# Kernel optimization log

Hardware: AMD Instinct MI355X
Metric: run time of the kernel (lower is better)

Reference implementation:

```python
import jax, jax.numpy as jnp
import numpy as np

TEMPERATURE = 0.6
REPETITION_PENALTY = 1.2
VOCAB = 50257


def setup_inputs() -> dict:
    key = jax.random.key(0)
    k1, k2 = jax.random.split(key)
    logits = jax.random.normal(k1, (8, 64, VOCAB), dtype=jnp.float32)
    prev_tokens = jax.random.randint(k2, (64, 200), 0, VOCAB, dtype=jnp.int64)
    return {"logits": logits, "prev_tokens": prev_tokens}


def reference(logits, prev_tokens):
    # logits: [B, S, V]; prev_tokens: [S, P] token ids previously generated per sequence.
    B, S, V = logits.shape
    # set-semantics mask of penalized (seq, token) pairs; duplicate ids collapse to one.
    mask = jnp.zeros((S, V), dtype=bool).at[
        jnp.arange(S)[:, None], prev_tokens
    ].set(True)  # [S, V]
    # torch.all over dim 0: penalty multiplies if all batch logits negative, else divides.
    all_neg = jnp.all(logits < 0, axis=0, keepdims=True)  # [1, S, V]
    penalized = jnp.where(all_neg, logits * REPETITION_PENALTY, logits / REPETITION_PENALTY)
    logits = jnp.where(mask[None, :, :], penalized, logits)
    # Categorical(logits=x) -> probs = softmax(x); temperature scaling fused.
    return jax.nn.softmax(logits / TEMPERATURE, axis=-1)
```

## Files before the change

kernel.cpp:

```cpp
#include <hip/hip_runtime.h>
#include <math.h>

#define BB 8
#define SS 64
#define VV 50257
#define PP 200
#define NMASK 1571
#define NT 1024
#define ITER 13
constexpr float RP   = 1.2f;
constexpr float TINV = 1.0f / 0.6f;

__global__ __launch_bounds__(NT) void sch_fused_kernel(
        const float* __restrict__ logits,
        const int*   __restrict__ prev,
        float*       __restrict__ out) {
    __shared__ unsigned mask[NMASK];
    __shared__ float ss[16];
    __shared__ float bc_li;

    const int bs  = blockIdx.x;
    const int s   = bs & (SS - 1);
    const int tid = threadIdx.x;
    const float* row  = logits + (size_t)bs * VV;
    float*       orow = out    + (size_t)bs * VV;

    for (int i = tid; i < NMASK; i += NT) mask[i] = 0u;
    __syncthreads();

    float delta  = 0.0f;
    float eadj   = 0.0f;
    int   vtok   = -1;
    bool  winner = false;
    if (tid < PP) {
        vtok = prev[s * PP + tid];
        unsigned bit = 1u << (vtok & 31);
        unsigned old = atomicOr(&mask[vtok >> 5], bit);
        winner = (old & bit) == 0u;
        if (winner) {
            float lv[BB];
            bool all_neg = true;
            #pragma unroll
            for (int b = 0; b < BB; ++b) {
                lv[b] = logits[((size_t)(b * SS + s)) * VV + vtok];
                all_neg = all_neg && (lv[b] < 0.0f);
            }
            const float myraw = lv[bs >> 6];
            const float adj   = all_neg ? myraw * RP : myraw / RP;
            eadj  = __expf(adj * TINV);
            delta = eadj - __expf(myraw * TINV);
        }
    }

    const int a0   = (4 - (bs & 3)) & 3;
    const int nb   = (VV - a0) >> 2;
    const int tail = VV - a0 - (nb << 2);
    const int tstart = a0 + (nb << 2);

    const float4* body = (const float4*)(row + a0);
    float4 buf[ITER];
    #pragma unroll
    for (int k = 0; k < ITER; ++k) {
        int i = tid + k * NT;
        if (i < nb) buf[k] = body[i];
    }
    float escal = 0.0f;
    const bool has_head = (tid < a0);
    const bool has_tail = (tid >= 4 && tid < 4 + tail);
    if (has_head) escal = __expf(row[tid] * TINV);
    if (has_tail) escal = __expf(row[tstart + tid - 4] * TINV);

    float4 acc = make_float4(0.f, 0.f, 0.f, 0.f);
    #pragma unroll
    for (int k = 0; k < ITER; ++k) {
        int i = tid + k * NT;
        if (i < nb) {
            float4 x = buf[k];
            float4 e;
            e.x = __expf(x.x * TINV);
            e.y = __expf(x.y * TINV);
            e.z = __expf(x.z * TINV);
            e.w = __expf(x.w * TINV);
            buf[k] = e;
            acc.x += e.x; acc.y += e.y; acc.z += e.z; acc.w += e.w;
        }
    }
    float sum = (acc.x + acc.y) + (acc.z + acc.w) + escal + delta;

    #pragma unroll
    for (int off = 1; off < 64; off <<= 1)
        sum += __shfl_xor(sum, off);
    const int wave = tid >> 6, lane = tid & 63;
    if (lane == 0) ss[wave] = sum;
    __syncthreads();
    if (tid == 0) {
        float S0 = ss[0];
        #pragma unroll
        for (int w = 1; w < 16; ++w) S0 += ss[w];
        bc_li = 1.0f / S0;
    }
    __syncthreads();
    const float li = bc_li;

    float4* obody = (float4*)(orow + a0);
    #pragma unroll
    for (int k = 0; k < ITER; ++k) {
        int i = tid + k * NT;
        if (i < nb) {
            float4 e = buf[k];
            obody[i] = make_float4(e.x * li, e.y * li, e.z * li, e.w * li);
        }
    }
    if (has_head) orow[tid]               = escal * li;
    if (has_tail) orow[tstart + tid - 4]  = escal * li;

    __syncthreads();
    if (winner) orow[vtok] = eadj * li;
}

extern "C" void kernel_launch(void* const* d_in, const int* in_sizes, int n_in,
                              void* d_out, int out_size, void* d_ws, size_t ws_size,
                              hipStream_t stream) {
    const float* logits = (const float*)d_in[0];
    const int*   prev   = (const int*)d_in[1];
    float* out = (float*)d_out;

    sch_fused_kernel<<<BB * SS, NT, 0, stream>>>(logits, prev, out);
}
```

Measured before the change: 187.3 us.

## Hoist row and penalty-token loads before mask setup, use nontemporal output stores

Issues the bulk row loads and the eight gathered batch logits per previous token before the mask clear and atomic dedup, so their latency overlaps the shared-memory setup and barrier. Output writes now use nontemporal stores to avoid polluting cache with streaming data. The launch bounds gain a min-blocks hint and float4 is replaced by an ext_vector type. The gathers now run for every token thread rather than only dedup winners, which adds redundant loads, and the occupancy hint may constrain register allocation.

```diff
diff --git a/kernel.cpp b/kernel.cpp
--- a/kernel.cpp
+++ b/kernel.cpp
@@ -11,7 +11,9 @@
 constexpr float RP   = 1.2f;
 constexpr float TINV = 1.0f / 0.6f;
 
-__global__ __launch_bounds__(NT) void sch_fused_kernel(
+typedef float f32x4 __attribute__((ext_vector_type(4)));
+
+__global__ __launch_bounds__(NT, 4) void sch_fused_kernel(
         const float* __restrict__ logits,
         const int*   __restrict__ prev,
         float*       __restrict__ out) {
@@ -25,26 +27,46 @@
     const float* row  = logits + (size_t)bs * VV;
     float*       orow = out    + (size_t)bs * VV;
 
+    const int a0   = (4 - (bs & 3)) & 3;
+    const int nb   = (VV - a0) >> 2;
+    const int tail = VV - a0 - (nb << 2);
+    const int tstart = a0 + (nb << 2);
+
+    const f32x4* body = (const f32x4*)(row + a0);
+    f32x4 buf[ITER];
+    #pragma unroll
+    for (int k = 0; k < ITER; ++k) {
+        int i = tid + k * NT;
+        if (i < nb) buf[k] = body[i];
+    }
+    float xscal = 0.0f;
+    const bool has_head = (tid < a0);
+    const bool has_tail = (tid >= 4 && tid < 4 + tail);
+    if (has_head) xscal = row[tid];
+    if (has_tail) xscal = row[tstart + tid - 4];
+
+    int   vtok = -1;
+    float lv[BB];
+    if (tid < PP) {
+        vtok = prev[s * PP + tid];
+        #pragma unroll
+        for (int b = 0; b < BB; ++b)
+            lv[b] = logits[((size_t)(b * SS + s)) * VV + vtok];
+    }
     for (int i = tid; i < NMASK; i += NT) mask[i] = 0u;
     __syncthreads();
 
     float delta  = 0.0f;
     float eadj   = 0.0f;
-    int   vtok   = -1;
     bool  winner = false;
     if (tid < PP) {
-        vtok = prev[s * PP + tid];
         unsigned bit = 1u << (vtok & 31);
         unsigned old = atomicOr(&mask[vtok >> 5], bit);
         winner = (old & bit) == 0u;
         if (winner) {
-            float lv[BB];
             bool all_neg = true;
             #pragma unroll
-            for (int b = 0; b < BB; ++b) {
-                lv[b] = logits[((size_t)(b * SS + s)) * VV + vtok];
-                all_neg = all_neg && (lv[b] < 0.0f);
-            }
+            for (int b = 0; b < BB; ++b) all_neg = all_neg && (lv[b] < 0.0f);
             const float myraw = lv[bs >> 6];
             const float adj   = all_neg ? myraw * RP : myraw / RP;
             eadj  = __expf(adj * TINV);
@@ -52,40 +74,23 @@
         }
     }
 
-    const int a0   = (4 - (bs & 3)) & 3;
-    const int nb   = (VV - a0) >> 2;
-    const int tail = VV - a0 - (nb << 2);
-    const int tstart = a0 + (nb << 2);
-
-    const float4* body = (const float4*)(row + a0);
-    float4 buf[ITER];
-    #pragma unroll
-    for (int k = 0; k < ITER; ++k) {
-        int i = tid + k * NT;
-        if (i < nb) buf[k] = body[i];
-    }
-    float escal = 0.0f;
-    const bool has_head = (tid < a0);
-    const bool has_tail = (tid >= 4 && tid < 4 + tail);
-    if (has_head) escal = __expf(row[tid] * TINV);
-    if (has_tail) escal = __expf(row[tstart + tid - 4] * TINV);
-
-    float4 acc = make_float4(0.f, 0.f, 0.f, 0.f);
+    float escal = (has_head || has_tail) ? __expf(xscal * TINV) : 0.0f;
+    float accx = 0.f, accy = 0.f, accz = 0.f, accw = 0.f;
     #pragma unroll
     for (int k = 0; k < ITER; ++k) {
         int i = tid + k * NT;
         if (i < nb) {
-            float4 x = buf[k];
-            float4 e;
+            f32x4 x = buf[k];
+            f32x4 e;
             e.x = __expf(x.x * TINV);
             e.y = __expf(x.y * TINV);
             e.z = __expf(x.z * TINV);
             e.w = __expf(x.w * TINV);
             buf[k] = e;
-            acc.x += e.x; acc.y += e.y; acc.z += e.z; acc.w += e.w;
+            accx += e.x; accy += e.y; accz += e.z; accw += e.w;
         }
     }
-    float sum = (acc.x + acc.y) + (acc.z + acc.w) + escal + delta;
+    float sum = (accx + accy) + (accz + accw) + escal + delta;
 
     #pragma unroll
     for (int off = 1; off < 64; off <<= 1)
@@ -102,17 +107,19 @@
     __syncthreads();
     const float li = bc_li;
 
-    float4* obody = (float4*)(orow + a0);
+    f32x4* obody = (f32x4*)(orow + a0);
     #pragma unroll
     for (int k = 0; k < ITER; ++k) {
         int i = tid + k * NT;
         if (i < nb) {
-            float4 e = buf[k];
-            obody[i] = make_float4(e.x * li, e.y * li, e.z * li, e.w * li);
+            f32x4 e = buf[k];
+            f32x4 o;
+            o.x = e.x * li; o.y = e.y * li; o.z = e.z * li; o.w = e.w * li;
+            __builtin_nontemporal_store(o, &obody[i]);
         }
     }
-    if (has_head) orow[tid]               = escal * li;
-    if (has_tail) orow[tstart + tid - 4]  = escal * li;
+    if (has_head) __builtin_nontemporal_store(escal * li, &orow[tid]);
+    if (has_tail) __builtin_nontemporal_store(escal * li, &orow[tstart + tid - 4]);
 
     __syncthreads();
     if (winner) orow[vtok] = eadj * li;
```

New measurement: 194.8 us. 1.04x slower.
